# Kernel tuning notes

Hardware: AMD Instinct MI355X
Metric: run time of the kernel (lower is better)

The kernel has to match this reference:

```python
import jax, jax.numpy as jnp
import numpy as np
import math

CHUNK = 128


def setup_inputs() -> dict:
    key = jax.random.key(0)
    ks = jax.random.split(key, 12)
    B, S, H, D = 2, 4096, 1024, 2048  # D = hidden_dim * expansion_factor
    std = 0.02
    inp = {
        "hidden_states": jax.random.normal(ks[0], (B, S, H), jnp.float32),
        "Wq": jax.random.normal(ks[1], (H, D), jnp.float32) * std,
        "bq": jnp.zeros((D,), jnp.float32),
        "Wk": jax.random.normal(ks[2], (H, D), jnp.float32) * std,
        "bk": jnp.zeros((D,), jnp.float32),
        "Wv": jax.random.normal(ks[3], (H, D), jnp.float32) * std,
        "bv": jnp.zeros((D,), jnp.float32),
        "Wg": jax.random.normal(ks[4], (H, D), jnp.float32) * std,
        "bg": jnp.zeros((D,), jnp.float32),
        "Wo": jax.random.normal(ks[5], (D, H), jnp.float32) * std,
        "bo": jnp.zeros((H,), jnp.float32),
    }
    return inp


def reference(hidden_states, Wq, bq, Wk, bk, Wv, bv, Wg, bg, Wo, bo):
    B, S, H = hidden_states.shape
    D = Wq.shape[1]
    cs = CHUNK
    nC = S // cs  # seq_len chosen as multiple of chunk_size (no padding path)

    q = hidden_states @ Wq + bq
    k = hidden_states @ Wk + bk
    v = hidden_states @ Wv + bv
    gate = jax.nn.sigmoid(hidden_states @ Wg + bg)

    qc = q.reshape(B, nC, cs, D)
    kc = k.reshape(B, nC, cs, D)
    vc = v.reshape(B, nC, cs, D)
    gc = gate.reshape(B, nC, cs, D)

    # intra-chunk causal softmax attention (vectorized over all chunks)
    scale = 1.0 / math.sqrt(D)
    attn = jnp.einsum('bncd,bnkd->bnck', qc, kc) * scale  # [B,nC,cs,cs]
    causal = jnp.tril(jnp.ones((cs, cs), bool))
    attn = jnp.where(causal, attn, -jnp.inf)
    attn = jax.nn.softmax(attn, axis=-1)
    local = jnp.einsum('bnck,bnkd->bncd', attn, vc)

    # inter-chunk linear-attention state accumulation:
    # cross_i = q_i @ sum_{j<i} K_j^T V_j  (sequential scan over chunks)
    def step(state, xs):
        qi, ki, vi = xs  # each [B,cs,D]
        cross = jnp.einsum('bcd,bde->bce', qi, state)
        state = state + jnp.einsum('bcd,bce->bde', ki, vi)
        return state, cross

    state0 = jnp.zeros((B, D, D), hidden_states.dtype)
    _, cross = jax.lax.scan(
        step, state0,
        (qc.transpose(1, 0, 2, 3), kc.transpose(1, 0, 2, 3), vc.transpose(1, 0, 2, 3)))
    cross = cross.transpose(1, 0, 2, 3)  # [B,nC,cs,D]

    out = (local + cross) * gc
    out = out.reshape(B, S, D)
    return out @ Wo + bo
```

## Files before the change

### kernel.cpp

```cpp
#include <hip/hip_runtime.h>
#include <hip/hip_bf16.h>
#include <math.h>


typedef __bf16 bf16_t;
typedef __bf16 bf16x8 __attribute__((ext_vector_type(8)));
typedef __bf16 bf16x4 __attribute__((ext_vector_type(4)));
typedef float f32x4 __attribute__((ext_vector_type(4)));

#define NB_ 2
#define SEQ 4096
#define HID 1024
#define DD 2048
#define BS 8192
#define LDS_CORE 98304
#define SP 264

__device__ __forceinline__ void async16(const void* g, void* l) {
  __builtin_amdgcn_global_load_lds(
      (const __attribute__((address_space(1))) void*)g,
      (__attribute__((address_space(3))) void*)l, 16, 0, 0);
}

#define VMW(n) asm volatile("s_waitcnt vmcnt(" #n ")" ::: "memory")
#define BARR __builtin_amdgcn_s_barrier()
#define FEN asm volatile("" ::: "memory")

template <int MFH>
__device__ __forceinline__ void readA8(const bf16_t* bufA, int aBase, int s0, int s1,
                                       bf16x8 (&af)[4][2]) {
#pragma unroll
  for (int mm = 0; mm < 4; ++mm) {
    int p = aBase + MFH * 8192 + mm * 1024;
    af[mm][0] = *reinterpret_cast<const bf16x8*>(&bufA[p + s0]);
    af[mm][1] = *reinterpret_cast<const bf16x8*>(&bufA[p + s1]);
  }
}
template <int NFH>
__device__ __forceinline__ void readB4(const bf16_t* bufB, int bBase, int s0, int s1,
                                       bf16x8 (&bv)[2][2]) {
#pragma unroll
  for (int nn = 0; nn < 2; ++nn) {
    int p = bBase + NFH * 8192 + nn * 1024;
    bv[nn][0] = *reinterpret_cast<const bf16x8*>(&bufB[p + s0]);
    bv[nn][1] = *reinterpret_cast<const bf16x8*>(&bufB[p + s1]);
  }
}
template <int MROWS, int MQ, int NQ>
__device__ __forceinline__ void mfmaQ(const bf16x8 (&af)[4][2], const bf16x8 (&bv)[2][2],
                                      f32x4 (&acc)[MROWS][4]) {
  __builtin_amdgcn_s_setprio(1);
#pragma unroll
  for (int kki = 0; kki < 2; ++kki)
#pragma unroll
    for (int mm = 0; mm < 4; ++mm)
#pragma unroll
      for (int nn = 0; nn < 2; ++nn)
        acc[MQ * 4 + mm][NQ * 2 + nn] = __builtin_amdgcn_mfma_f32_16x16x32_bf16(
            af[mm][kki], bv[nn][kki], acc[MQ * 4 + mm][NQ * 2 + nn], 0, 0, 0);
  __builtin_amdgcn_s_setprio(0);
}

__device__ __forceinline__ void core128(const bf16_t* __restrict__ A, int lda,
                                        const bf16_t* __restrict__ B, int ldb, int nt,
                                        bf16_t* lds, f32x4 (&acc)[4][4]) {
  const int t = threadIdx.x;
  const int lane = t & 63, w = t >> 6;
  const int wm = w >> 2, wn = w & 3;
  const int lr = lane & 15, lg = lane >> 4;
  const int xm = lr & 7;
  const int aBase = (wm * 64 + lr) * 64;
  const int bBase = (wn * 32 + lr) * 64;
  const int s0 = (lg ^ xm) * 8, s1 = ((4 + lg) ^ xm) * 8;
  const int slog = ((t & 7) ^ ((t >> 3) & 7)) * 8;
  int srcA[2], srcB[4];
#pragma unroll
  for (int blk = 0; blk < 2; ++blk) srcA[blk] = (blk * 64 + (t >> 3)) * lda + slog;
#pragma unroll
  for (int blk = 0; blk < 4; ++blk) {
    int prB = (blk << 6) + (t >> 3);
    int rB = (((prB >> 5) & 3) << 6) + ((prB >> 7) << 5) + (prB & 31);
    srcB[blk] = rB * ldb + slog;
  }
  const int dstT = t * 8;
#pragma unroll
  for (int m = 0; m < 4; ++m)
#pragma unroll
    for (int n = 0; n < 4; ++n) acc[m][n] = (f32x4){0.f, 0.f, 0.f, 0.f};

  {
    bf16_t* nA = lds;
    bf16_t* nB = lds + 8192;
    async16(A + srcA[0], nA + dstT);
    async16(A + srcA[1], nA + 4096 + dstT);
    async16(B + srcB[0], nB + dstT);
    async16(B + srcB[1], nB + 4096 + dstT);
    async16(B + srcB[2], nB + 8192 + dstT);
    async16(B + srcB[3], nB + 12288 + dstT);
  }
  bf16x8 af[4][2], bv0[2][2], bv1[2][2];
  for (int kt = 0; kt < nt; ++kt) {
    bf16_t* bufA = lds + (kt & 1) * 24576;
    bf16_t* bufB = bufA + 8192;
    bf16_t* nA = lds + ((kt + 1) & 1) * 24576;
    bf16_t* nB = nA + 8192;
    const int kn = (kt + 1 < nt ? kt + 1 : 0) << 6;
    const bf16_t* An = A + kn;
    const bf16_t* Bn = B + kn;
    VMW(2); BARR; FEN;
    readA8<0>(bufA, aBase, s0, s1, af);
    readB4<0>(bufB, bBase, s0, s1, bv0);
    async16(An + srcA[0], nA + dstT);
    async16(An + srcA[1], nA + 4096 + dstT);
    async16(Bn + srcB[0], nB + dstT);
    mfmaQ<4, 0, 0>(af, bv0, acc);
    VMW(3); BARR; FEN;
    readB4<1>(bufB, bBase, s0, s1, bv1);
    async16(Bn + srcB[1], nB + 4096 + dstT);
    async16(Bn + srcB[2], nB + 8192 + dstT);
    async16(Bn + srcB[3], nB + 12288 + dstT);
    mfmaQ<4, 0, 1>(af, bv1, acc);
  }
  VMW(0);
  BARR;
}

__global__ void k_cvt(const float4* __restrict__ in, bf16x4* __restrict__ out, int n4) {
  int i = blockIdx.x * blockDim.x + threadIdx.x;
  if (i < n4) {
    float4 v = in[i];
    bf16x4 o;
    o[0] = (bf16_t)v.x; o[1] = (bf16_t)v.y; o[2] = (bf16_t)v.z; o[3] = (bf16_t)v.w;
    out[i] = o;
  }
}

__global__ void k_tconv(const float* __restrict__ in, bf16_t* __restrict__ out,
                        int R, int C) {
  __shared__ bf16_t tile[64][65];
  int bc = blockIdx.x, br = blockIdx.y;
  int t = threadIdx.x;
  int c = t & 63, r0 = t >> 6;
#pragma unroll
  for (int rr = 0; rr < 64; rr += 4) {
    int r = rr + r0;
    tile[r][c] = (bf16_t)in[(long)(br * 64 + r) * C + bc * 64 + c];
  }
  __syncthreads();
#pragma unroll
  for (int rr = 0; rr < 64; rr += 4) {
    int r = rr + r0;
    out[(long)(bc * 64 + r) * R + br * 64 + c] = tile[c][r];
  }
}

__global__ void k_tbf16(const bf16_t* __restrict__ in, bf16_t* __restrict__ out,
                        int R, int C) {
  __shared__ bf16_t tile[64][65];
  long zoff = (long)blockIdx.z * R * C;
  in += zoff;
  out += zoff;
  int bc = blockIdx.x, br = blockIdx.y;
  int t = threadIdx.x;
  int c = t & 63, r0 = t >> 6;
#pragma unroll
  for (int rr = 0; rr < 64; rr += 4) {
    int r = rr + r0;
    tile[r][c] = in[(long)(br * 64 + r) * C + bc * 64 + c];
  }
  __syncthreads();
#pragma unroll
  for (int rr = 0; rr < 64; rr += 4) {
    int r = rr + r0;
    out[(long)(bc * 64 + r) * R + br * 64 + c] = tile[c][r];
  }
}

__global__ __launch_bounds__(512, 2) void k_gemm_qkvg(
    const bf16_t* __restrict__ hsb, const bf16_t* __restrict__ Wt4,
    const float* __restrict__ bq, const float* __restrict__ bk,
    const float* __restrict__ bv, const float* __restrict__ bg,
    bf16_t* __restrict__ out) {
  extern __shared__ bf16_t lds[];
  int c = blockIdx.x;
  int r = c >> 9, xj = c & 511;
  int xcd = xj & 7, j = xj >> 3;
  int mb = r * 16 + (xcd & 1) * 8 + (j & 7);
  int nb = (xcd >> 1) * 8 + (j >> 3);
  f32x4 acc[4][4];
  core128(hsb + (long)mb * 128 * HID, HID, Wt4 + (long)nb * 256 * HID, HID,
          HID / 64, lds, acc);
  const int t = threadIdx.x, lane = t & 63, w = t >> 6;
  const int wm = w >> 2, wn = w & 3, lr = lane & 15, lg = lane >> 4;
  int z = nb >> 3;
  const float* bias = z == 0 ? bq : z == 1 ? bk : z == 2 ? bv : bg;
  int colT = (nb & 7) * 256;
  float b4[4];
#pragma unroll
  for (int nf = 0; nf < 4; ++nf) b4[nf] = bias[colT + wn * 64 + nf * 16 + lr];
#pragma unroll
  for (int mf = 0; mf < 4; ++mf)
#pragma unroll
    for (int reg = 0; reg < 4; ++reg) {
      int lrow = wm * 64 + mf * 16 + lg * 4 + reg;
#pragma unroll
      for (int nf = 0; nf < 4; ++nf) {
        float v = acc[mf][nf][reg] + b4[nf];
        if (z == 3) v = 1.f / (1.f + __expf(-v));
        lds[lrow * SP + wn * 64 + nf * 16 + lr] = (bf16_t)v;
      }
    }
  __syncthreads();
  bf16_t* O = out + (long)z * BS * DD + (long)mb * 128 * DD + colT;
#pragma unroll
  for (int it = 0; it < 8; ++it) {
    int s = it * 512 + t;
    int rr2 = s >> 5, sg = s & 31;
    bf16x8 v = *reinterpret_cast<const bf16x8*>(&lds[rr2 * SP + sg * 8]);
    *reinterpret_cast<bf16x8*>(&O[(long)rr2 * DD + sg * 8]) = v;
  }
}

__global__ __launch_bounds__(512, 2) void k_pair(const bf16_t* __restrict__ Q,
                                                 const bf16_t* __restrict__ Kb,
                                                 bf16_t* __restrict__ P) {
  extern __shared__ bf16_t lds[];
  int p = blockIdx.x, b = blockIdx.y;
  int c = 0, base = 0;
  while (base + (c >> 1) + 1 <= p) { base += (c >> 1) + 1; ++c; }
  int jt = p - base;
  f32x4 acc[4][4];
  core128(Q + ((long)b * SEQ + (long)c * 128) * DD, DD,
          Kb + ((long)b * SEQ + (long)jt * 256) * DD, DD, DD / 64, lds, acc);
  const int t = threadIdx.x, lane = t & 63, w = t >> 6;
  const int wm = w >> 2, wn = w & 3, lr = lane & 15, lg = lane >> 4;
  bf16_t* Pt = P + ((long)b * SEQ + (long)c * 128) * (long)SEQ + (long)jt * 256;
  const bool hasDiag = (jt == (c >> 1));
  const int side = c & 1;
  const float scale = 0.02209708691207961f;
#pragma unroll
  for (int mf = 0; mf < 4; ++mf)
#pragma unroll
    for (int reg = 0; reg < 4; ++reg) {
      int lrow = wm * 64 + mf * 16 + lg * 4 + reg;
#pragma unroll
      for (int nf = 0; nf < 4; ++nf) {
        int col = wn * 64 + nf * 16 + lr;
        float v = acc[mf][nf][reg];
        if (hasDiag && (((col >> 7) == side) || side == 0)) v = 0.f;
        lds[lrow * SP + col] = (bf16_t)v;
      }
    }
  __syncthreads();
#pragma unroll
  for (int it = 0; it < 8; ++it) {
    int s = it * 512 + t;
    int rr2 = s >> 5, sg = s & 31;
    bf16x8 v = *reinterpret_cast<const bf16x8*>(&lds[rr2 * SP + sg * 8]);
    *reinterpret_cast<bf16x8*>(&Pt[(long)rr2 * SEQ + sg * 8]) = v;
  }
  if (hasDiag) {
    VMW(0);
    __syncthreads();
    float* smf = (float*)lds;
#pragma unroll
    for (int mf = 0; mf < 4; ++mf)
#pragma unroll
      for (int reg = 0; reg < 4; ++reg) {
        int row = wm * 64 + mf * 16 + lg * 4 + reg;
#pragma unroll
        for (int nf = 0; nf < 4; ++nf) {
          int col = wn * 64 + nf * 16 + lr;
          if ((col >> 7) == side) {
            int cc = col & 127;
            float sv = acc[mf][nf][reg] * scale;
            smf[row * 128 + ((cc + row) & 127)] = (cc <= row) ? sv : -1e30f;
          }
        }
      }
    __syncthreads();
    if (t < 128) {
      int r = t;
      float mx = -1e30f;
      for (int cc = 0; cc <= r; ++cc) mx = fmaxf(mx, smf[r * 128 + ((cc + r) & 127)]);
      float s = 0.f;
      for (int cc = 0; cc <= r; ++cc) s += __expf(smf[r * 128 + ((cc + r) & 127)] - mx);
      float inv = 1.f / s;
      for (int cc = 0; cc < 128; ++cc) {
        float v = (cc <= r) ? __expf(smf[r * 128 + ((cc + r) & 127)] - mx) * inv : 0.f;
        Pt[(long)r * SEQ + side * 128 + cc] = (bf16_t)v;
      }
    }
  }
}

__global__ __launch_bounds__(512, 2) void k_gemm2(const bf16_t* __restrict__ P,
                                                  const bf16_t* __restrict__ Vt,
                                                  const bf16_t* __restrict__ G,
                                                  bf16_t* __restrict__ OutPre) {
  extern __shared__ bf16_t lds[];
  int bid = blockIdx.x;
  int mq = 31 - (bid >> 4);
  int r2 = bid & 15;
  int nb = r2 >> 1, b = r2 & 1;
  f32x4 acc[4][4];
  core128(P + ((long)b * SEQ + (long)mq * 128) * (long)SEQ, SEQ,
          Vt + (long)b * DD * SEQ + (long)nb * 256 * SEQ, SEQ, (mq + 1) * 2, lds, acc);
  const int t = threadIdx.x, lane = t & 63, w = t >> 6;
  const int wm = w >> 2, wn = w & 3, lr = lane & 15, lg = lane >> 4;
  long rowb = (long)b * SEQ + (long)mq * 128;
#pragma unroll
  for (int mf = 0; mf < 4; ++mf)
#pragma unroll
    for (int reg = 0; reg < 4; ++reg) {
      int lrow = wm * 64 + mf * 16 + lg * 4 + reg;
#pragma unroll
      for (int nf = 0; nf < 4; ++nf) {
        int col = wn * 64 + nf * 16 + lr;
        float g = (float)G[(rowb + lrow) * DD + nb * 256 + col];
        lds[lrow * SP + col] = (bf16_t)(acc[mf][nf][reg] * g);
      }
    }
  __syncthreads();
  bf16_t* O = OutPre + rowb * DD + nb * 256;
#pragma unroll
  for (int it = 0; it < 8; ++it) {
    int s = it * 512 + t;
    int rr2 = s >> 5, sg = s & 31;
    bf16x8 v = *reinterpret_cast<const bf16x8*>(&lds[rr2 * SP + sg * 8]);
    *reinterpret_cast<bf16x8*>(&O[(long)rr2 * DD + sg * 8]) = v;
  }
}

__global__ __launch_bounds__(512, 2) void k_gemm3(const bf16_t* __restrict__ OutPre,
                                                  const bf16_t* __restrict__ Wot,
                                                  const float* __restrict__ bo,
                                                  float* __restrict__ out) {
  extern __shared__ bf16_t lds[];
  int mb = blockIdx.x >> 2, nb = blockIdx.x & 3;
  f32x4 acc[4][4];
  core128(OutPre + (long)mb * 128 * DD, DD, Wot + (long)nb * 256 * DD, DD,
          DD / 64, lds, acc);
  const int t = threadIdx.x, lane = t & 63, w = t >> 6;
  const int wm = w >> 2, wn = w & 3, lr = lane & 15, lg = lane >> 4;
  int colbase = nb * 256 + wn * 64;
  float b4[4];
#pragma unroll
  for (int nf = 0; nf < 4; ++nf) b4[nf] = bo[colbase + nf * 16 + lr];
#pragma unroll
  for (int mf = 0; mf < 4; ++mf)
#pragma unroll
    for (int reg = 0; reg < 4; ++reg) {
      long row = mb * 128 + wm * 64 + mf * 16 + lg * 4 + reg;
#pragma unroll
      for (int nf = 0; nf < 4; ++nf)
        out[row * HID + colbase + nf * 16 + lr] = acc[mf][nf][reg] + b4[nf];
    }
}

extern "C" void kernel_launch(void* const* d_in, const int* in_sizes, int n_in,
                              void* d_out, int out_size, void* d_ws, size_t ws_size,
                              hipStream_t stream) {
  const float* hs = (const float*)d_in[0];
  const float* Wq = (const float*)d_in[1];
  const float* bq = (const float*)d_in[2];
  const float* Wk = (const float*)d_in[3];
  const float* bk = (const float*)d_in[4];
  const float* Wv = (const float*)d_in[5];
  const float* bv = (const float*)d_in[6];
  const float* Wg = (const float*)d_in[7];
  const float* bg = (const float*)d_in[8];
  const float* Wo = (const float*)d_in[9];
  const float* bo = (const float*)d_in[10];
  float* out = (float*)d_out;

  char* ws = (char*)d_ws;
  const size_t MB = 1024 * 1024;
  bf16_t* P = (bf16_t*)(ws);
  bf16_t* hsb = (bf16_t*)(ws);
  bf16_t* Wt4 = (bf16_t*)(ws + 16 * MB);
  bf16_t* Wot = (bf16_t*)(ws + 64 * MB);
  bf16_t* QKVG = (bf16_t*)(ws + 68 * MB);
  bf16_t* Vt = (bf16_t*)(ws + 196 * MB);

  bf16_t* Qb = QKVG;
  bf16_t* Kbuf = QKVG + (long)BS * DD;
  bf16_t* Vbuf = QKVG + 2l * BS * DD;
  bf16_t* Gbuf = QKVG + 3l * BS * DD;
  bf16_t* OutPre = Vbuf;

  hipFuncSetAttribute((const void*)k_gemm_qkvg,
                      hipFuncAttributeMaxDynamicSharedMemorySize, LDS_CORE);
  hipFuncSetAttribute((const void*)k_pair,
                      hipFuncAttributeMaxDynamicSharedMemorySize, LDS_CORE);
  hipFuncSetAttribute((const void*)k_gemm2,
                      hipFuncAttributeMaxDynamicSharedMemorySize, LDS_CORE);
  hipFuncSetAttribute((const void*)k_gemm3,
                      hipFuncAttributeMaxDynamicSharedMemorySize, LDS_CORE);

  k_cvt<<<(BS * HID / 4 + 255) / 256, 256, 0, stream>>>((const float4*)hs,
                                                        (bf16x4*)hsb, BS * HID / 4);
  k_tconv<<<dim3(DD / 64, HID / 64), 256, 0, stream>>>(Wq, Wt4 + 0l * DD * HID, HID, DD);
  k_tconv<<<dim3(DD / 64, HID / 64), 256, 0, stream>>>(Wk, Wt4 + 1l * DD * HID, HID, DD);
  k_tconv<<<dim3(DD / 64, HID / 64), 256, 0, stream>>>(Wv, Wt4 + 2l * DD * HID, HID, DD);
  k_tconv<<<dim3(DD / 64, HID / 64), 256, 0, stream>>>(Wg, Wt4 + 3l * DD * HID, HID, DD);
  k_tconv<<<dim3(HID / 64, DD / 64), 256, 0, stream>>>(Wo, Wot, DD, HID);

  k_gemm_qkvg<<<2048, 512, LDS_CORE, stream>>>(hsb, Wt4, bq, bk, bv, bg, QKVG);

  k_tbf16<<<dim3(DD / 64, SEQ / 64, NB_), 256, 0, stream>>>(Vbuf, Vt, SEQ, DD);

  k_pair<<<dim3(272, 2), 512, LDS_CORE, stream>>>(Qb, Kbuf, P);

  k_gemm2<<<512, 512, LDS_CORE, stream>>>(P, Vt, Gbuf, OutPre);

  k_gemm3<<<256, 512, LDS_CORE, stream>>>(OutPre, Wot, bo, out);
}
```

Before: 446.6 us.

## Fuse V transpose into QKVG GEMM with new K32 core and direct epilogues

Adds a new double-buffered K=32 GEMM core with swizzled LDS layout and uses it for the QKVG projection with 256x128 tiles, smaller LDS and higher occupancy. The V projection epilogue now writes V directly in transposed layout, which removes the separate k_tbf16 transpose kernel and its extra round trip through memory. The k_pair and k_gemm2 epilogues write results straight to global memory instead of staging them through LDS, removing a barrier and the LDS pass. The direct stores are scattered 2-byte writes rather than coalesced 16-byte vectors, which may cost memory efficiency.

```diff
diff --git a/kernel.cpp b/kernel.cpp
--- a/kernel.cpp
+++ b/kernel.cpp
@@ -13,8 +13,8 @@
 #define HID 1024
 #define DD 2048
 #define BS 8192
-#define LDS_CORE 98304
-#define SP 264
+#define LDS_128 98304
+#define LDS_QKVG 69632
 
 __device__ __forceinline__ void async16(const void* g, void* l) {
   __builtin_amdgcn_global_load_lds(
@@ -23,6 +23,7 @@
 }
 
 #define VMW(n) asm volatile("s_waitcnt vmcnt(" #n ")" ::: "memory")
+#define VMW0 asm volatile("s_waitcnt vmcnt(0)" ::: "memory")
 #define BARR __builtin_amdgcn_s_barrier()
 #define FEN asm volatile("" ::: "memory")
 
@@ -121,8 +122,80 @@
     async16(Bn + srcB[3], nB + 12288 + dstT);
     mfmaQ<4, 0, 1>(af, bv1, acc);
   }
-  VMW(0);
+  VMW0;
   BARR;
+}
+
+template <int WM, int WN>
+__device__ __forceinline__ void coreK32(const bf16_t* __restrict__ A, int lda,
+                                        const bf16_t* __restrict__ B, int ldb, int nt,
+                                        bf16_t* lds, f32x4 (&acc)[4][4]) {
+  constexpr int T = WM * WN * 64;
+  constexpr int AE = WM * 64 * 32;
+  constexpr int BUF = AE + WN * 64 * 32;
+  constexpr int NISS = BUF / (T * 8);
+  const int t = threadIdx.x;
+  const int lane = t & 63, w = t >> 6;
+  const int wm = w / WN, wn = w % WN;
+  const int lr = lane & 15, lg = lane >> 4;
+
+  int aOff[4], bOff[4];
+#pragma unroll
+  for (int f = 0; f < 4; ++f) {
+    int ra = wm * 64 + f * 16 + lr;
+    aOff[f] = ra * 32 + (((lg + (ra >> 1)) & 3) << 3);
+    int rb = wn * 64 + f * 16 + lr;
+    bOff[f] = AE + rb * 32 + (((lg + (rb >> 1)) & 3) << 3);
+  }
+  int src[NISS];
+#pragma unroll
+  for (int q = 0; q < NISS; ++q) {
+    int e = q * T * 8 + t * 8;
+    bool isB = (q * T * 8) >= AE;
+    int e2 = isB ? e - AE : e;
+    int r = e2 >> 5;
+    int g = (((e2 >> 3) & 3) - (r >> 1)) & 3;
+    src[q] = r * (isB ? ldb : lda) + g * 8;
+  }
+#pragma unroll
+  for (int m = 0; m < 4; ++m)
+#pragma unroll
+    for (int n = 0; n < 4; ++n) acc[m][n] = (f32x4){0.f, 0.f, 0.f, 0.f};
+
+  {
+    bf16_t* buf0 = lds;
+#pragma unroll
+    for (int q = 0; q < NISS; ++q) {
+      bool isB = (q * T * 8) >= AE;
+      async16((isB ? B : A) + src[q], buf0 + q * T * 8 + t * 8);
+    }
+  }
+  VMW0; BARR; FEN;
+
+  for (int tt = 0; tt < nt; ++tt) {
+    bf16_t* cur = lds + (tt & 1) * BUF;
+    bf16_t* nxt = lds + ((tt + 1) & 1) * BUF;
+    const int kn = (tt + 1 < nt ? tt + 1 : 0) << 5;
+#pragma unroll
+    for (int q = 0; q < NISS; ++q) {
+      bool isB = (q * T * 8) >= AE;
+      async16((isB ? B : A) + kn + src[q], nxt + q * T * 8 + t * 8);
+    }
+    bf16x8 af[4], bv[4];
+#pragma unroll
+    for (int f = 0; f < 4; ++f) af[f] = *reinterpret_cast<const bf16x8*>(&cur[aOff[f]]);
+#pragma unroll
+    for (int f = 0; f < 4; ++f) bv[f] = *reinterpret_cast<const bf16x8*>(&cur[bOff[f]]);
+    __builtin_amdgcn_s_setprio(1);
+#pragma unroll
+    for (int mf = 0; mf < 4; ++mf)
+#pragma unroll
+      for (int nf = 0; nf < 4; ++nf)
+        acc[mf][nf] =
+            __builtin_amdgcn_mfma_f32_16x16x32_bf16(af[mf], bv[nf], acc[mf][nf], 0, 0, 0);
+    __builtin_amdgcn_s_setprio(0);
+    VMW0; BARR; FEN;
+  }
 }
 
 __global__ void k_cvt(const float4* __restrict__ in, bf16x4* __restrict__ out, int n4) {
@@ -154,70 +227,73 @@
   }
 }
 
-__global__ void k_tbf16(const bf16_t* __restrict__ in, bf16_t* __restrict__ out,
-                        int R, int C) {
-  __shared__ bf16_t tile[64][65];
-  long zoff = (long)blockIdx.z * R * C;
-  in += zoff;
-  out += zoff;
-  int bc = blockIdx.x, br = blockIdx.y;
-  int t = threadIdx.x;
-  int c = t & 63, r0 = t >> 6;
-#pragma unroll
-  for (int rr = 0; rr < 64; rr += 4) {
-    int r = rr + r0;
-    tile[r][c] = in[(long)(br * 64 + r) * C + bc * 64 + c];
-  }
-  __syncthreads();
-#pragma unroll
-  for (int rr = 0; rr < 64; rr += 4) {
-    int r = rr + r0;
-    out[(long)(bc * 64 + r) * R + br * 64 + c] = tile[c][r];
-  }
-}
-
-__global__ __launch_bounds__(512, 2) void k_gemm_qkvg(
+__global__ __launch_bounds__(512, 4) void k_gemm_qkvg(
     const bf16_t* __restrict__ hsb, const bf16_t* __restrict__ Wt4,
     const float* __restrict__ bq, const float* __restrict__ bk,
     const float* __restrict__ bv, const float* __restrict__ bg,
-    bf16_t* __restrict__ out) {
+    bf16_t* __restrict__ out, bf16_t* __restrict__ Vt) {
   extern __shared__ bf16_t lds[];
-  int c = blockIdx.x;
-  int r = c >> 9, xj = c & 511;
-  int xcd = xj & 7, j = xj >> 3;
-  int mb = r * 16 + (xcd & 1) * 8 + (j & 7);
-  int nb = (xcd >> 1) * 8 + (j >> 3);
+  const int SP = 136;
+  const int SPT = 264;
+  int i = blockIdx.x;
+  int xcd = i & 7, g = i >> 3;
+  int mb = g >> 3;
+  int nb = xcd * 8 + (g & 7);
   f32x4 acc[4][4];
-  core128(hsb + (long)mb * 128 * HID, HID, Wt4 + (long)nb * 256 * HID, HID,
-          HID / 64, lds, acc);
+  coreK32<4, 2>(hsb + (long)mb * 256 * HID, HID, Wt4 + (long)nb * 128 * HID, HID,
+                HID / 32, lds, acc);
   const int t = threadIdx.x, lane = t & 63, w = t >> 6;
-  const int wm = w >> 2, wn = w & 3, lr = lane & 15, lg = lane >> 4;
-  int z = nb >> 3;
+  const int wm = w >> 1, wn = w & 1, lr = lane & 15, lg = lane >> 4;
+  int z = nb >> 4;
   const float* bias = z == 0 ? bq : z == 1 ? bk : z == 2 ? bv : bg;
-  int colT = (nb & 7) * 256;
+  int colT = (nb & 15) * 128;
   float b4[4];
 #pragma unroll
   for (int nf = 0; nf < 4; ++nf) b4[nf] = bias[colT + wn * 64 + nf * 16 + lr];
-#pragma unroll
-  for (int mf = 0; mf < 4; ++mf)
-#pragma unroll
-    for (int reg = 0; reg < 4; ++reg) {
-      int lrow = wm * 64 + mf * 16 + lg * 4 + reg;
-#pragma unroll
-      for (int nf = 0; nf < 4; ++nf) {
-        float v = acc[mf][nf][reg] + b4[nf];
-        if (z == 3) v = 1.f / (1.f + __expf(-v));
-        lds[lrow * SP + wn * 64 + nf * 16 + lr] = (bf16_t)v;
+  if (z != 2) {
+#pragma unroll
+    for (int mf = 0; mf < 4; ++mf)
+#pragma unroll
+      for (int reg = 0; reg < 4; ++reg) {
+        int lrow = wm * 64 + mf * 16 + lg * 4 + reg;
+#pragma unroll
+        for (int nf = 0; nf < 4; ++nf) {
+          float v = acc[mf][nf][reg] + b4[nf];
+          if (z == 3) v = 1.f / (1.f + __expf(-v));
+          lds[lrow * SP + wn * 64 + nf * 16 + lr] = (bf16_t)v;
+        }
       }
-    }
-  __syncthreads();
-  bf16_t* O = out + (long)z * BS * DD + (long)mb * 128 * DD + colT;
-#pragma unroll
-  for (int it = 0; it < 8; ++it) {
-    int s = it * 512 + t;
-    int rr2 = s >> 5, sg = s & 31;
-    bf16x8 v = *reinterpret_cast<const bf16x8*>(&lds[rr2 * SP + sg * 8]);
-    *reinterpret_cast<bf16x8*>(&O[(long)rr2 * DD + sg * 8]) = v;
+    __syncthreads();
+    bf16_t* O = out + (long)z * BS * DD + (long)mb * 256 * DD + colT;
+#pragma unroll
+    for (int it = 0; it < 8; ++it) {
+      int s = it * 512 + t;
+      int row = s >> 4, sg = s & 15;
+      bf16x8 v = *reinterpret_cast<const bf16x8*>(&lds[row * SP + sg * 8]);
+      *reinterpret_cast<bf16x8*>(&O[(long)row * DD + sg * 8]) = v;
+    }
+  } else {
+#pragma unroll
+    for (int mf = 0; mf < 4; ++mf)
+#pragma unroll
+      for (int reg = 0; reg < 4; ++reg) {
+        int lrow = wm * 64 + mf * 16 + lg * 4 + reg;
+#pragma unroll
+        for (int nf = 0; nf < 4; ++nf) {
+          int d = wn * 64 + nf * 16 + lr;
+          lds[d * SPT + lrow] = (bf16_t)(acc[mf][nf][reg] + b4[nf]);
+        }
+      }
+    __syncthreads();
+    int bz = mb >> 4, smb = mb & 15;
+    bf16_t* Vd = Vt + ((long)bz * DD + colT) * SEQ + smb * 256;
+#pragma unroll
+    for (int it = 0; it < 8; ++it) {
+      int s = it * 512 + t;
+      int d = s >> 5, sg = s & 31;
+      bf16x8 v = *reinterpret_cast<const bf16x8*>(&lds[d * SPT + sg * 8]);
+      *reinterpret_cast<bf16x8*>(&Vd[(long)d * SEQ + sg * 8]) = v;
+    }
   }
 }
 
@@ -238,46 +314,27 @@
   const bool hasDiag = (jt == (c >> 1));
   const int side = c & 1;
   const float scale = 0.02209708691207961f;
+  float* smf = (float*)lds;
 #pragma unroll
   for (int mf = 0; mf < 4; ++mf)
 #pragma unroll
     for (int reg = 0; reg < 4; ++reg) {
-      int lrow = wm * 64 + mf * 16 + lg * 4 + reg;
+      int row = wm * 64 + mf * 16 + lg * 4 + reg;
 #pragma unroll
       for (int nf = 0; nf < 4; ++nf) {
         int col = wn * 64 + nf * 16 + lr;
         float v = acc[mf][nf][reg];
-        if (hasDiag && (((col >> 7) == side) || side == 0)) v = 0.f;
-        lds[lrow * SP + col] = (bf16_t)v;
-      }
-    }
-  __syncthreads();
-#pragma unroll
-  for (int it = 0; it < 8; ++it) {
-    int s = it * 512 + t;
-    int rr2 = s >> 5, sg = s & 31;
-    bf16x8 v = *reinterpret_cast<const bf16x8*>(&lds[rr2 * SP + sg * 8]);
-    *reinterpret_cast<bf16x8*>(&Pt[(long)rr2 * SEQ + sg * 8]) = v;
-  }
-  if (hasDiag) {
-    VMW(0);
-    __syncthreads();
-    float* smf = (float*)lds;
-#pragma unroll
-    for (int mf = 0; mf < 4; ++mf)
-#pragma unroll
-      for (int reg = 0; reg < 4; ++reg) {
-        int row = wm * 64 + mf * 16 + lg * 4 + reg;
-#pragma unroll
-        for (int nf = 0; nf < 4; ++nf) {
-          int col = wn * 64 + nf * 16 + lr;
-          if ((col >> 7) == side) {
-            int cc = col & 127;
-            float sv = acc[mf][nf][reg] * scale;
-            smf[row * 128 + ((cc + row) & 127)] = (cc <= row) ? sv : -1e30f;
-          }
+        if (hasDiag && ((col >> 7) == side)) {
+          int cc = col & 127;
+          float sv = v * scale;
+          smf[row * 128 + ((cc + row) & 127)] = (cc <= row) ? sv : -1e30f;
+        } else {
+          if (hasDiag && side == 0 && (col >> 7) == 1) v = 0.f;
+          Pt[(long)row * SEQ + col] = (bf16_t)v;
         }
       }
+    }
+  if (hasDiag) {
     __syncthreads();
     if (t < 128) {
       int r = t;
@@ -308,28 +365,18 @@
           Vt + (long)b * DD * SEQ + (long)nb * 256 * SEQ, SEQ, (mq + 1) * 2, lds, acc);
   const int t = threadIdx.x, lane = t & 63, w = t >> 6;
   const int wm = w >> 2, wn = w & 3, lr = lane & 15, lg = lane >> 4;
-  long rowb = (long)b * SEQ + (long)mq * 128;
 #pragma unroll
   for (int mf = 0; mf < 4; ++mf)
 #pragma unroll
     for (int reg = 0; reg < 4; ++reg) {
-      int lrow = wm * 64 + mf * 16 + lg * 4 + reg;
+      long row = (long)b * SEQ + (long)mq * 128 + wm * 64 + mf * 16 + lg * 4 + reg;
 #pragma unroll
       for (int nf = 0; nf < 4; ++nf) {
-        int col = wn * 64 + nf * 16 + lr;
-        float g = (float)G[(rowb + lrow) * DD + nb * 256 + col];
-        lds[lrow * SP + col] = (bf16_t)(acc[mf][nf][reg] * g);
+        long idx = row * DD + nb * 256 + wn * 64 + nf * 16 + lr;
+        float g = (float)G[idx];
+        OutPre[idx] = (bf16_t)(acc[mf][nf][reg] * g);
       }
     }
-  __syncthreads();
-  bf16_t* O = OutPre + rowb * DD + nb * 256;
-#pragma unroll
-  for (int it = 0; it < 8; ++it) {
-    int s = it * 512 + t;
-    int rr2 = s >> 5, sg = s & 31;
-    bf16x8 v = *reinterpret_cast<const bf16x8*>(&lds[rr2 * SP + sg * 8]);
-    *reinterpret_cast<bf16x8*>(&O[(long)rr2 * DD + sg * 8]) = v;
-  }
 }
 
 __global__ __launch_bounds__(512, 2) void k_gemm3(const bf16_t* __restrict__ OutPre,
@@ -390,13 +437,13 @@
   bf16_t* OutPre = Vbuf;
 
   hipFuncSetAttribute((const void*)k_gemm_qkvg,
-                      hipFuncAttributeMaxDynamicSharedMemorySize, LDS_CORE);
+                      hipFuncAttributeMaxDynamicSharedMemorySize, LDS_QKVG);
   hipFuncSetAttribute((const void*)k_pair,
-                      hipFuncAttributeMaxDynamicSharedMemorySize, LDS_CORE);
+                      hipFuncAttributeMaxDynamicSharedMemorySize, LDS_128);
   hipFuncSetAttribute((const void*)k_gemm2,
-                      hipFuncAttributeMaxDynamicSharedMemorySize, LDS_CORE);
+                      hipFuncAttributeMaxDynamicSharedMemorySize, LDS_128);
   hipFuncSetAttribute((const void*)k_gemm3,
-                      hipFuncAttributeMaxDynamicSharedMemorySize, LDS_CORE);
+                      hipFuncAttributeMaxDynamicSharedMemorySize, LDS_128);
 
   k_cvt<<<(BS * HID / 4 + 255) / 256, 256, 0, stream>>>((const float4*)hs,
                                                         (bf16x4*)hsb, BS * HID / 4);
@@ -406,13 +453,11 @@
   k_tconv<<<dim3(DD / 64, HID / 64), 256, 0, stream>>>(Wg, Wt4 + 3l * DD * HID, HID, DD);
   k_tconv<<<dim3(HID / 64, DD / 64), 256, 0, stream>>>(Wo, Wot, DD, HID);
 
-  k_gemm_qkvg<<<2048, 512, LDS_CORE, stream>>>(hsb, Wt4, bq, bk, bv, bg, QKVG);
-
-  k_tbf16<<<dim3(DD / 64, SEQ / 64, NB_), 256, 0, stream>>>(Vbuf, Vt, SEQ, DD);
-
-  k_pair<<<dim3(272, 2), 512, LDS_CORE, stream>>>(Qb, Kbuf, P);
-
-  k_gemm2<<<512, 512, LDS_CORE, stream>>>(P, Vt, Gbuf, OutPre);
-
-  k_gemm3<<<256, 512, LDS_CORE, stream>>>(OutPre, Wot, bo, out);
-}
+  k_gemm_qkvg<<<2048, 512, LDS_QKVG, stream>>>(hsb, Wt4, bq, bk, bv, bg, QKVG, Vt);
+
+  k_pair<<<dim3(272, 2), 512, LDS_128, stream>>>(Qb, Kbuf, P);
+
+  k_gemm2<<<512, 512, LDS_128, stream>>>(P, Vt, Gbuf, OutPre);
+
+  k_gemm3<<<256, 512, LDS_128, stream>>>(OutPre, Wot, bo, out);
+}
```

New measurement: 421.9 us (median of 2 runs). 5.5% less time.
